# Kernel tuning notes

Measured on AMD Instinct MI355X. Metric: run time of the kernel, lower is better.

Reference implementation:

```python
import jax, jax.numpy as jnp
import numpy as np

T = 256        # number of save/step points
BATCH = 2048   # batched trajectories
DATA = 32      # state dim (data_size)
WIDTH = 128    # MLP width
DELAYS = (1.0, 2.0)  # constant delays tau_j (all >> dt so lookups are in the past)


def setup_inputs() -> dict:
    key = jax.random.key(0)
    ks = jax.random.split(key, 5)
    ts = jnp.linspace(0.0, 10.0, T, dtype=jnp.float32)
    y0 = jax.random.normal(ks[0], (BATCH, DATA), dtype=jnp.float32)
    in_size = (len(DELAYS) + 1) * DATA  # (nb_delays + 1) * data_size

    def lin(k, o, i):
        kw, kb = jax.random.split(k)
        lim = 1.0 / np.sqrt(i)
        W = jax.random.uniform(kw, (o, i), jnp.float32, -lim, lim)
        b = jax.random.uniform(kb, (o,), jnp.float32, -lim, lim)
        return W, b

    W0, b0 = lin(ks[1], WIDTH, in_size)   # in -> width
    W1, b1 = lin(ks[2], WIDTH, WIDTH)     # hidden
    W2, b2 = lin(ks[3], WIDTH, WIDTH)     # hidden
    W3, b3 = lin(ks[4], DATA, WIDTH)      # width -> out (no activation)
    return dict(ts=ts, y0=y0, W0=W0, b0=b0, W1=W1, b1=b1, W2=W2, b2=b2, W3=W3, b3=b3)


def _mlp(x, W0, b0, W1, b1, W2, b2, W3, b3):
    # eqx.nn.MLP(depth=3, activation=relu): 4 linears, relu after hidden layers
    h = jax.nn.relu(x @ W0.T + b0)
    h = jax.nn.relu(h @ W1.T + b1)
    h = jax.nn.relu(h @ W2.T + b2)
    return h @ W3.T + b3


def _solve(ts, y0, params):
    t0 = ts[0]
    dt0 = ts[1] - ts[0]

    def lookup(buf, t):
        # linear interpolation of stored history on the uniform grid;
        # t <= t0 clips to index 0 where buf[0] == y0 (constant initial history)
        s = jnp.clip((t - t0) / dt0, 0.0, T - 1.0)
        i0 = jnp.floor(s).astype(jnp.int32)
        i1 = jnp.minimum(i0 + 1, T - 1)
        w = s - i0.astype(s.dtype)
        return (1.0 - w) * buf[i0] + w * buf[i1]

    def f(t, y, buf):
        hist = [lookup(buf, t - tau) for tau in DELAYS]
        return _mlp(jnp.concatenate([y] + hist, axis=-1), *params)

    buf0 = jnp.zeros((T, BATCH, DATA), y0.dtype).at[0].set(y0)

    def step(carry, inp):
        y, buf = carry
        i, t, t_next = inp
        dt = t_next - t
        # Bosh3 / Bogacki-Shampine stages
        k1 = f(t, y, buf)
        k2 = f(t + 0.5 * dt, y + 0.5 * dt * k1, buf)
        k3 = f(t + 0.75 * dt, y + 0.75 * dt * k2, buf)
        y_next = y + dt * (2.0 / 9.0 * k1 + 1.0 / 3.0 * k2 + 4.0 / 9.0 * k3)
        buf = buf.at[i + 1].set(y_next)
        return (y_next, buf), y_next

    xs = (jnp.arange(T - 1), ts[:-1], ts[1:])
    (_, _), ys_tail = jax.lax.scan(step, (y0, buf0), xs)
    return jnp.concatenate([y0[None], ys_tail], axis=0)  # [T, BATCH, DATA]


def reference(ts, y0, W0, b0, W1, b1, W2, b2, W3, b3):
    ys = _solve(ts, y0, (W0, b0, W1, b1, W2, b2, W3, b3))
    return ys, jnp.int32(T - 1)  # (solution.ys, num_steps)
```

## Files before the change

### kernel.cpp

```cpp
#include <hip/hip_runtime.h>

#define TT 256
#define BATCH 2048
#define DATA 32
#define WSLOTS 52

typedef __bf16 bf16x8 __attribute__((ext_vector_type(8)));
typedef float f32x4 __attribute__((ext_vector_type(4)));

#define MFMA(A, B, C) __builtin_amdgcn_mfma_f32_16x16x32_bf16((A), (B), (C), 0, 0, 0)

union bfp2 { uint2 u; __bf16 b[4]; };
union bfp4 { uint4 q; bf16x8 v; __bf16 b[8]; };

__device__ __forceinline__ bf16x8 ldw8(const float* __restrict__ p) {
    float4 a = *(const float4*)p;
    float4 b = *(const float4*)(p + 4);
    bf16x8 r;
    r[0] = (__bf16)a.x; r[1] = (__bf16)a.y; r[2] = (__bf16)a.z; r[3] = (__bf16)a.w;
    r[4] = (__bf16)b.x; r[5] = (__bf16)b.y; r[6] = (__bf16)b.z; r[7] = (__bf16)b.w;
    return r;
}

__device__ __forceinline__ bf16x8 ldx(const char* base, int row, int kbyte) {
    return *(const bf16x8*)(base + row * 256 + (kbyte ^ ((row & 7) << 4)));
}

#define HID2(WF, KC, SRC, DST, BI0, BI1)                                              \
    {                                                                                 \
        bf16x8 xf[4];                                                                 \
        _Pragma("unroll") for (int kc = 0; kc < (KC); ++kc)                           \
            xf[kc] = ldx(SRC, m, kc * 64 + g * 16);                                   \
        f32x4 a0 = BI0, a1 = BI1;                                                     \
        _Pragma("unroll") for (int kc = 0; kc < (KC); ++kc) {                         \
            a0 = MFMA(WF[0][kc], xf[kc], a0);                                         \
            a1 = MFMA(WF[1][kc], xf[kc], a1);                                         \
        }                                                                             \
        bfp2 p0, p1;                                                                  \
        _Pragma("unroll") for (int j = 0; j < 4; ++j) {                               \
            p0.b[j] = (__bf16)fmaxf(a0[j], 0.0f);                                     \
            p1.b[j] = (__bf16)fmaxf(a1[j], 0.0f);                                     \
        }                                                                             \
        char* dr = (DST) + m * 256;                                                   \
        *(uint2*)(dr + ((tbB + g * 8) ^ sw)) = p0.u;                                  \
        *(uint2*)(dr + ((tbB + 32 + g * 8) ^ sw)) = p1.u;                             \
    }

#define PRELERP(TQT, XDST)                                                            \
    {                                                                                 \
        const int   dl  = wv - 2;                                                     \
        const float tau = dl ? 2.0f : 1.0f;                                           \
        float s = ((TQT) - tau - t0v) * ivd0;                                         \
        s = fminf(fmaxf(s, 0.0f), 255.0f);                                            \
        const int   i0 = (int)s;                                                      \
        const int   i1 = min(i0 + 1, TT - 1);                                         \
        const float w  = s - (float)i0;                                               \
        bfp4 pa, pb, pr;                                                              \
        pa.v = *(const bf16x8*)(hists + (i0 % WSLOTS) * 1280 + m * 80 + g * 16);      \
        pb.v = *(const bf16x8*)(hists + (i1 % WSLOTS) * 1280 + m * 80 + g * 16);      \
        _Pragma("unroll") for (int e = 0; e < 8; ++e) {                               \
            const float va = (float)pa.b[e];                                          \
            pr.b[e] = (__bf16)fmaf(w, (float)pb.b[e] - va, va);                       \
        }                                                                             \
        *(bf16x8*)((XDST) + dl * 1280 + m * 80 + g * 16) = pr.v;                      \
    }

#define DO_STAGE(USEK, CST, KP, KD, XSRC, XDST, TQT)                                  \
    {                                                                                 \
            \
        bfp4 xf0;                                                                     \
        _Pragma("unroll") for (int e = 0; e < 8; ++e)                                 \
            xf0.b[e] = (__bf16)((USEK) ? fmaf((CST) * dt, KP[e], y[e]) : y[e]);       \
        bf16x8 xl1 = *(const bf16x8*)((XSRC) + m * 80 + g * 16);                      \
        bf16x8 xl2 = *(const bf16x8*)((XSRC) + 1280 + m * 80 + g * 16);               \
        f32x4 a0 = bias0[0], a1 = bias0[1];                                           \
        a0 = MFMA(W0f[0][0], xf0.v, a0); a1 = MFMA(W0f[1][0], xf0.v, a1);             \
        a0 = MFMA(W0f[0][1], xl1, a0);   a1 = MFMA(W0f[1][1], xl1, a1);               \
        a0 = MFMA(W0f[0][2], xl2, a0);   a1 = MFMA(W0f[1][2], xl2, a1);               \
        bfp2 p0, p1;                                                                  \
        _Pragma("unroll") for (int j = 0; j < 4; ++j) {                               \
            p0.b[j] = (__bf16)fmaxf(a0[j], 0.0f);                                     \
            p1.b[j] = (__bf16)fmaxf(a1[j], 0.0f);                                     \
        }                                                                             \
        char* dr = hA + m * 256;                                                      \
        *(uint2*)(dr + ((tbB + g * 8) ^ sw)) = p0.u;                                  \
        *(uint2*)(dr + ((tbB + 32 + g * 8) ^ sw)) = p1.u;                             \
        __syncthreads();                                                              \
        HID2(W1f, 4, hA, hB, bias1[0], bias1[1])                                      \
        __syncthreads();                                                              \
        HID2(W2f, 4, hB, hA, bias2[0], bias2[1])                                      \
        __syncthreads();                                                              \
        if (wv < 2) {                      \
            bf16x8 xf[4];                                                             \
            _Pragma("unroll") for (int kc = 0; kc < 4; ++kc)                          \
                xf[kc] = ldx(hA, m, kc * 64 + g * 16);                                \
            f32x4 a = bias3;                                                          \
            _Pragma("unroll") for (int kc = 0; kc < 4; ++kc)                          \
                a = MFMA(W3f[kc], xf[kc], a);                                         \
            *(f32x4*)(kbuf + m * 128 + (((wv * 4 + g) ^ (m & 7)) << 4)) = a;          \
        } else {                                                                      \
            PRELERP(TQT, XDST)                                                        \
        }                                                                             \
        __syncthreads();                                                              \
        {                           \
            f32x4 q0 = *(const f32x4*)(kbuf + m * 128 + (((2 * g) ^ (m & 7)) << 4));  \
            f32x4 q1 = *(const f32x4*)(kbuf + m * 128 + (((2 * g + 1) ^ (m & 7)) << 4)); \
            _Pragma("unroll") for (int j = 0; j < 4; ++j) {                           \
                KD[j] = q0[j]; KD[4 + j] = q1[j];                                     \
            }                                                                         \
        }                                                                             \
    }

__global__ __launch_bounds__(256, 1) void dde_m(
    const float* __restrict__ ts, const float* __restrict__ y0,
    const float* __restrict__ W0, const float* __restrict__ b0,
    const float* __restrict__ W1, const float* __restrict__ b1,
    const float* __restrict__ W2, const float* __restrict__ b2,
    const float* __restrict__ W3, const float* __restrict__ b3,
    float* __restrict__ out)
{
    __shared__ __align__(16) char hists[WSLOTS * 1280];
    __shared__ __align__(16) char xb0[2 * 1280];
    __shared__ __align__(16) char xb1[2 * 1280];
    __shared__ __align__(16) char xb2[2 * 1280];
    __shared__ __align__(16) char hA[16 * 256];
    __shared__ __align__(16) char hB[16 * 256];
    __shared__ __align__(16) char kbuf[16 * 128];
    __shared__ float tsb[TT];

    const int tid  = threadIdx.x;
    const int lane = tid & 63;
    const int wv   = tid >> 6;
    const int m    = lane & 15;
    const int g    = lane >> 4;
    const int tbB  = wv * 64;
    const int sw   = (m & 7) << 4;
    const int R0   = blockIdx.x * 16;

    for (int idx = tid; idx < WSLOTS * 320; idx += 256) ((unsigned*)hists)[idx] = 0u;
    for (int idx = tid; idx < TT; idx += 256) tsb[idx] = ts[idx];

    bf16x8 W0f[2][3], W1f[2][4], W2f[2][4], W3f[4];
    #pragma unroll
    for (int ti = 0; ti < 2; ++ti) {
        const int rw = (wv * 2 + ti) * 16 + m;
        #pragma unroll
        for (int kc = 0; kc < 3; ++kc) W0f[ti][kc] = ldw8(W0 + rw * 96 + kc * 32 + g * 8);
        #pragma unroll
        for (int kc = 0; kc < 4; ++kc) W1f[ti][kc] = ldw8(W1 + rw * 128 + kc * 32 + g * 8);
        #pragma unroll
        for (int kc = 0; kc < 4; ++kc) W2f[ti][kc] = ldw8(W2 + rw * 128 + kc * 32 + g * 8);
    }
    {
        const int rw3 = (wv & 1) * 16 + m;
        #pragma unroll
        for (int kc = 0; kc < 4; ++kc) W3f[kc] = ldw8(W3 + rw3 * 128 + kc * 32 + g * 8);
    }
    f32x4 bias0[2], bias1[2], bias2[2], bias3;
    #pragma unroll
    for (int ti = 0; ti < 2; ++ti) {
        bias0[ti] = *(const f32x4*)(b0 + (wv * 2 + ti) * 16 + g * 4);
        bias1[ti] = *(const f32x4*)(b1 + (wv * 2 + ti) * 16 + g * 4);
        bias2[ti] = *(const f32x4*)(b2 + (wv * 2 + ti) * 16 + g * 4);
    }
    bias3 = *(const f32x4*)(b3 + (wv & 1) * 16 + g * 4);

    __syncthreads();

    float y[8], k1[8], k2[8], k3[8];
    {
        float4 v0 = *(const float4*)(y0 + (R0 + m) * DATA + g * 8);
        float4 v1 = *(const float4*)(y0 + (R0 + m) * DATA + g * 8 + 4);
        y[0] = v0.x; y[1] = v0.y; y[2] = v0.z; y[3] = v0.w;
        y[4] = v1.x; y[5] = v1.y; y[6] = v1.z; y[7] = v1.w;
        #pragma unroll
        for (int e = 0; e < 8; ++e) { k1[e] = 0.0f; k2[e] = 0.0f; k3[e] = 0.0f; }
        if (wv == 0) {
            bfp4 p;
            #pragma unroll
            for (int e = 0; e < 8; ++e) p.b[e] = (__bf16)y[e];
            *(bf16x8*)(hists + m * 80 + g * 16) = p.v;
            *(float4*)(out + (R0 + m) * DATA + g * 8) = v0;
            *(float4*)(out + (R0 + m) * DATA + g * 8 + 4) = v1;
        }
    }
    if (blockIdx.x == 0 && tid == 0)
        out[(size_t)TT * BATCH * DATA] = 255.0f;
    __syncthreads();

    const float t0v  = tsb[0];
    const float ivd0 = 1.0f / (tsb[1] - tsb[0]);

    if (wv >= 2) {
        const float dt0 = tsb[1] - tsb[0];
        PRELERP(t0v, xb0)
        PRELERP(fmaf(0.5f, dt0, t0v), xb1)
        PRELERP(fmaf(0.75f, dt0, t0v), xb2)
    }
    __syncthreads();

    #pragma unroll 1
    for (int i = 0; i < TT - 1; ++i) {
        const float t   = tsb[i];
        const float tn  = tsb[i + 1];
        const float dt  = tn - t;
        const float tnn = tsb[min(i + 2, TT - 1)];
        const float dtn = tnn - tn;

        DO_STAGE(0, 0.0f,  k1, k1, xb0, xb2, fmaf(0.75f, dt, t))
        DO_STAGE(1, 0.5f,  k1, k2, xb1, xb0, tn)
        DO_STAGE(2, 0.75f, k2, k3, xb2, xb1, fmaf(0.5f, dtn, tn))

        {
            #pragma unroll
            for (int e = 0; e < 8; ++e) {
                const float ks = (2.0f / 9.0f) * k1[e] + (1.0f / 3.0f) * k2[e]
                               + (4.0f / 9.0f) * k3[e];
                y[e] = fmaf(dt, ks, y[e]);
            }
            if (wv == 0) {
                bfp4 p;
                #pragma unroll
                for (int e = 0; e < 8; ++e) p.b[e] = (__bf16)y[e];
                *(bf16x8*)(hists + ((i + 1) % WSLOTS) * 1280 + m * 80 + g * 16) = p.v;
                float4 o0, o1;
                o0.x = y[0]; o0.y = y[1]; o0.z = y[2]; o0.w = y[3];
                o1.x = y[4]; o1.y = y[5]; o1.z = y[6]; o1.w = y[7];
                float* op = out + (size_t)(i + 1) * BATCH * DATA + (R0 + m) * DATA + g * 8;
                *(float4*)op = o0;
                *(float4*)(op + 4) = o1;
            }
        }
    }
}

extern "C" void kernel_launch(void* const* d_in, const int* in_sizes, int n_in,
                              void* d_out, int out_size, void* d_ws, size_t ws_size,
                              hipStream_t stream) {
    const float* ts = (const float*)d_in[0];
    const float* y0 = (const float*)d_in[1];
    const float* W0 = (const float*)d_in[2];
    const float* b0 = (const float*)d_in[3];
    const float* W1 = (const float*)d_in[4];
    const float* b1 = (const float*)d_in[5];
    const float* W2 = (const float*)d_in[6];
    const float* b2 = (const float*)d_in[7];
    const float* W3 = (const float*)d_in[8];
    const float* b3 = (const float*)d_in[9];

    dde_m<<<dim3(BATCH / 16), dim3(256), 0, stream>>>(
        ts, y0, W0, b0, W1, b1, W2, b2, W3, b3, (float*)d_out);
}
```

Baseline: 727.8 us.

## Split MLP output tiles across eight waves per block instead of four

The block grows from 4 to 8 waves, and each wave now computes one 16-row output tile of every hidden layer instead of two. The serial MFMA chain per wave per layer is halved, aiming to shorten the latency of each synchronised RK stage. In exchange there are more waves per barrier and each one does less work, and the upper waves sit idle during the output and lerp phase.

```diff
diff --git a/kernel.cpp b/kernel.cpp
--- a/kernel.cpp
+++ b/kernel.cpp
@@ -26,24 +26,18 @@
     return *(const bf16x8*)(base + row * 256 + (kbyte ^ ((row & 7) << 4)));
 }
 
-#define HID2(WF, KC, SRC, DST, BI0, BI1)                                              \
+#define HID1(WF, KC, SRC, DST, BI)                                                    \
     {                                                                                 \
         bf16x8 xf[4];                                                                 \
         _Pragma("unroll") for (int kc = 0; kc < (KC); ++kc)                           \
             xf[kc] = ldx(SRC, m, kc * 64 + g * 16);                                   \
-        f32x4 a0 = BI0, a1 = BI1;                                                     \
-        _Pragma("unroll") for (int kc = 0; kc < (KC); ++kc) {                         \
-            a0 = MFMA(WF[0][kc], xf[kc], a0);                                         \
-            a1 = MFMA(WF[1][kc], xf[kc], a1);                                         \
-        }                                                                             \
-        bfp2 p0, p1;                                                                  \
-        _Pragma("unroll") for (int j = 0; j < 4; ++j) {                               \
+        f32x4 a0 = BI;                                                                \
+        _Pragma("unroll") for (int kc = 0; kc < (KC); ++kc)                           \
+            a0 = MFMA(WF[kc], xf[kc], a0);                                            \
+        bfp2 p0;                                                                      \
+        _Pragma("unroll") for (int j = 0; j < 4; ++j)                                 \
             p0.b[j] = (__bf16)fmaxf(a0[j], 0.0f);                                     \
-            p1.b[j] = (__bf16)fmaxf(a1[j], 0.0f);                                     \
-        }                                                                             \
-        char* dr = (DST) + m * 256;                                                   \
-        *(uint2*)(dr + ((tbB + g * 8) ^ sw)) = p0.u;                                  \
-        *(uint2*)(dr + ((tbB + 32 + g * 8) ^ sw)) = p1.u;                             \
+        *(uint2*)((DST) + m * 256 + ((tbB2 + g * 8) ^ sw)) = p0.u;                    \
     }
 
 #define PRELERP(TQT, XDST)                                                            \
@@ -67,28 +61,24 @@
 
 #define DO_STAGE(USEK, CST, KP, KD, XSRC, XDST, TQT)                                  \
     {                                                                                 \
-            \
+                                 \
         bfp4 xf0;                                                                     \
         _Pragma("unroll") for (int e = 0; e < 8; ++e)                                 \
             xf0.b[e] = (__bf16)((USEK) ? fmaf((CST) * dt, KP[e], y[e]) : y[e]);       \
         bf16x8 xl1 = *(const bf16x8*)((XSRC) + m * 80 + g * 16);                      \
         bf16x8 xl2 = *(const bf16x8*)((XSRC) + 1280 + m * 80 + g * 16);               \
-        f32x4 a0 = bias0[0], a1 = bias0[1];                                           \
-        a0 = MFMA(W0f[0][0], xf0.v, a0); a1 = MFMA(W0f[1][0], xf0.v, a1);             \
-        a0 = MFMA(W0f[0][1], xl1, a0);   a1 = MFMA(W0f[1][1], xl1, a1);               \
-        a0 = MFMA(W0f[0][2], xl2, a0);   a1 = MFMA(W0f[1][2], xl2, a1);               \
-        bfp2 p0, p1;                                                                  \
-        _Pragma("unroll") for (int j = 0; j < 4; ++j) {                               \
+        f32x4 a0 = bias0;                                                             \
+        a0 = MFMA(W0f[0], xf0.v, a0);                                                 \
+        a0 = MFMA(W0f[1], xl1, a0);                                                   \
+        a0 = MFMA(W0f[2], xl2, a0);                                                   \
+        bfp2 p0;                                                                      \
+        _Pragma("unroll") for (int j = 0; j < 4; ++j)                                 \
             p0.b[j] = (__bf16)fmaxf(a0[j], 0.0f);                                     \
-            p1.b[j] = (__bf16)fmaxf(a1[j], 0.0f);                                     \
-        }                                                                             \
-        char* dr = hA + m * 256;                                                      \
-        *(uint2*)(dr + ((tbB + g * 8) ^ sw)) = p0.u;                                  \
-        *(uint2*)(dr + ((tbB + 32 + g * 8) ^ sw)) = p1.u;                             \
-        __syncthreads();                                                              \
-        HID2(W1f, 4, hA, hB, bias1[0], bias1[1])                                      \
-        __syncthreads();                                                              \
-        HID2(W2f, 4, hB, hA, bias2[0], bias2[1])                                      \
+        *(uint2*)(hA + m * 256 + ((tbB2 + g * 8) ^ sw)) = p0.u;                       \
+        __syncthreads();                                                              \
+        HID1(W1f, 4, hA, hB, bias1)                                                   \
+        __syncthreads();                                                              \
+        HID1(W2f, 4, hB, hA, bias2)                                                   \
         __syncthreads();                                                              \
         if (wv < 2) {                      \
             bf16x8 xf[4];                                                             \
@@ -98,7 +88,7 @@
             _Pragma("unroll") for (int kc = 0; kc < 4; ++kc)                          \
                 a = MFMA(W3f[kc], xf[kc], a);                                         \
             *(f32x4*)(kbuf + m * 128 + (((wv * 4 + g) ^ (m & 7)) << 4)) = a;          \
-        } else {                                                                      \
+        } else if (wv < 4) {                                                          \
             PRELERP(TQT, XDST)                                                        \
         }                                                                             \
         __syncthreads();                                                              \
@@ -111,7 +101,7 @@
         }                                                                             \
     }
 
-__global__ __launch_bounds__(256, 1) void dde_m(
+__global__ __launch_bounds__(512, 1) void dde_8w(
     const float* __restrict__ ts, const float* __restrict__ y0,
     const float* __restrict__ W0, const float* __restrict__ b0,
     const float* __restrict__ W1, const float* __restrict__ b1,
@@ -133,36 +123,30 @@
     const int wv   = tid >> 6;
     const int m    = lane & 15;
     const int g    = lane >> 4;
-    const int tbB  = wv * 64;
+    const int tbB2 = wv * 32;
     const int sw   = (m & 7) << 4;
     const int R0   = blockIdx.x * 16;
 
-    for (int idx = tid; idx < WSLOTS * 320; idx += 256) ((unsigned*)hists)[idx] = 0u;
-    for (int idx = tid; idx < TT; idx += 256) tsb[idx] = ts[idx];
-
-    bf16x8 W0f[2][3], W1f[2][4], W2f[2][4], W3f[4];
-    #pragma unroll
-    for (int ti = 0; ti < 2; ++ti) {
-        const int rw = (wv * 2 + ti) * 16 + m;
-        #pragma unroll
-        for (int kc = 0; kc < 3; ++kc) W0f[ti][kc] = ldw8(W0 + rw * 96 + kc * 32 + g * 8);
-        #pragma unroll
-        for (int kc = 0; kc < 4; ++kc) W1f[ti][kc] = ldw8(W1 + rw * 128 + kc * 32 + g * 8);
-        #pragma unroll
-        for (int kc = 0; kc < 4; ++kc) W2f[ti][kc] = ldw8(W2 + rw * 128 + kc * 32 + g * 8);
-    }
+    for (int idx = tid; idx < WSLOTS * 320; idx += 512) ((unsigned*)hists)[idx] = 0u;
+    if (tid < TT) tsb[tid] = ts[tid];
+
+    bf16x8 W0f[3], W1f[4], W2f[4], W3f[4];
     {
+        const int rw = wv * 16 + m;
+        #pragma unroll
+        for (int kc = 0; kc < 3; ++kc) W0f[kc] = ldw8(W0 + rw * 96 + kc * 32 + g * 8);
+        #pragma unroll
+        for (int kc = 0; kc < 4; ++kc) W1f[kc] = ldw8(W1 + rw * 128 + kc * 32 + g * 8);
+        #pragma unroll
+        for (int kc = 0; kc < 4; ++kc) W2f[kc] = ldw8(W2 + rw * 128 + kc * 32 + g * 8);
         const int rw3 = (wv & 1) * 16 + m;
         #pragma unroll
         for (int kc = 0; kc < 4; ++kc) W3f[kc] = ldw8(W3 + rw3 * 128 + kc * 32 + g * 8);
     }
-    f32x4 bias0[2], bias1[2], bias2[2], bias3;
-    #pragma unroll
-    for (int ti = 0; ti < 2; ++ti) {
-        bias0[ti] = *(const f32x4*)(b0 + (wv * 2 + ti) * 16 + g * 4);
-        bias1[ti] = *(const f32x4*)(b1 + (wv * 2 + ti) * 16 + g * 4);
-        bias2[ti] = *(const f32x4*)(b2 + (wv * 2 + ti) * 16 + g * 4);
-    }
+    f32x4 bias0, bias1, bias2, bias3;
+    bias0 = *(const f32x4*)(b0 + wv * 16 + g * 4);
+    bias1 = *(const f32x4*)(b1 + wv * 16 + g * 4);
+    bias2 = *(const f32x4*)(b2 + wv * 16 + g * 4);
     bias3 = *(const f32x4*)(b3 + (wv & 1) * 16 + g * 4);
 
     __syncthreads();
@@ -191,7 +175,7 @@
     const float t0v  = tsb[0];
     const float ivd0 = 1.0f / (tsb[1] - tsb[0]);
 
-    if (wv >= 2) {
+    if (wv >= 2 && wv < 4) {
         const float dt0 = tsb[1] - tsb[0];
         PRELERP(t0v, xb0)
         PRELERP(fmaf(0.5f, dt0, t0v), xb1)
@@ -248,6 +232,6 @@
     const float* W3 = (const float*)d_in[8];
     const float* b3 = (const float*)d_in[9];
 
-    dde_m<<<dim3(BATCH / 16), dim3(256), 0, stream>>>(
+    dde_8w<<<dim3(BATCH / 16), dim3(512), 0, stream>>>(
         ts, y0, W0, b0, W1, b1, W2, b2, W3, b3, (float*)d_out);
 }
```

After: 717.6 us. No clear change (-1.4%).
